# Kernel optimization log

Measured on AMD Instinct MI355X. Metric: run time of the kernel, lower is better.

## Reference

```python
import jax, jax.numpy as jnp
import numpy as np

N = 20000   # nodes
E = 160000  # edges
D = 128     # out_dim == in_dim
H = 8       # heads
DK = D // H # 16


def setup_inputs() -> dict:
    key = jax.random.key(0)
    ks = jax.random.split(key, 16)
    f = lambda i, shape, s=1.0: jax.random.normal(ks[i], shape, dtype=jnp.float32) * s
    z = lambda shape: jnp.zeros(shape, dtype=jnp.float32)
    return {
        "x_txt": f(0, (N, D)), "x_img": f(1, (N, D)), "x_s": f(2, (N, D)),
        "Wk": f(3, (D, D), 0.05), "bk": z((D,)),
        "Wq": f(4, (D, D), 0.05), "bq": z((D,)),
        "Wv": f(5, (D, D), 0.05), "bv": z((D,)),
        "Wa": f(6, (D, D), 0.05), "ba": z((D,)),
        "rel_att": f(7, (H, DK, DK), 0.25),
        "rel_msg": f(8, (H, DK, DK), 0.25),
        "rel_pri": jnp.ones((H,), jnp.float32),
        "wm_txt": f(9, (H, DK, DK), 0.25),
        "wm_img": f(10, (H, DK, DK), 0.25),
        "wm_s": f(11, (H, DK, DK), 0.25),
        "skip": jnp.ones((1,), jnp.float32),
        "src": jax.random.randint(ks[12], (E,), 0, N),
        "dst": jax.random.randint(ks[13], (E,), 0, N),
    }


def reference(x_txt, x_img, x_s, Wk, bk, Wq, bq, Wv, bv, Wa, ba,
              rel_att, rel_msg, rel_pri, wm_txt, wm_img, wm_s, skip, src, dst):
    n_heads, dk = rel_att.shape[0], rel_att.shape[1]
    n_nodes = x_txt.shape[0]
    sqrt_dk = jnp.sqrt(jnp.asarray(dk, jnp.float32))

    def proj(x, W, b):
        return (x @ W + b).reshape(n_nodes, n_heads, dk)

    xs = (x_txt, x_img, x_s)
    k = [proj(x, Wk, bk)[src] for x in xs]  # [E,H,dk] gathered at src
    q = [proj(x, Wq, bq)[dst] for x in xs]  # [E,H,dk] gathered at dst
    v = [proj(x, Wv, bv)[src] for x in xs]

    # cross-modal lambda: per-edge modality alignment softmax (over the 3 modalities)
    wm = (wm_txt, wm_img, wm_s)
    lam_scores = jnp.stack(
        [jnp.einsum('ehd,hdf,ehf->eh', k[m], wm[m], q[m]) for m in range(3)], axis=0)
    lam = jax.nn.softmax(lam_scores, axis=0)  # [3,E,H]

    # edge attention logits (scaled *10 as in reduce_func) and relation-msg values
    att = [jnp.einsum('ehd,hdf,ehf->eh', k[m], rel_att, q[m]) * rel_pri / sqrt_dk * 10.0
           for m in range(3)]
    vmsg = [jnp.einsum('ehd,hdf->ehf', v[m], rel_msg) for m in range(3)]

    align = -(jnp.abs(att[0] - att[1]) + jnp.abs(att[0] - att[2])
              + jnp.abs(att[1] - att[2])) / 3.0

    def seg_softmax(x):  # softmax over edges sharing the same dst node
        m = jax.ops.segment_max(x, dst, num_segments=n_nodes)
        m = jnp.where(jnp.isfinite(m), m, 0.0)
        e = jnp.exp(x - m[dst])
        s = jax.ops.segment_sum(e, dst, num_segments=n_nodes)
        s = jnp.where(s == 0.0, 1.0, s)
        return e / s[dst]

    beta2 = seg_softmax(align)
    sm = [seg_softmax(a) for a in att]
    beta1 = sm[0] * lam[0] + sm[1] * lam[1] + sm[2] * lam[2]
    beta = seg_softmax(beta1 * beta2)  # [E,H]

    alpha = jax.nn.sigmoid(skip)  # [1]
    outs = []
    for m in range(3):
        h = jax.ops.segment_sum(beta[..., None] * vmsg[m], dst,
                                num_segments=n_nodes).reshape(n_nodes, -1)
        outs.append((h @ Wa + ba) * alpha + xs[m] * (1.0 - alpha))
    return tuple(outs)
```

## Files before the change

### kernel.cpp

```cpp
#include <hip/hip_runtime.h>

#define D 128
#define NH 8

typedef __bf16 bf16x8 __attribute__((ext_vector_type(8)));
typedef unsigned short ushortx8 __attribute__((ext_vector_type(8)));
typedef float floatx4 __attribute__((ext_vector_type(4)));

__device__ __forceinline__ float bf2f(unsigned short u) {
  union { unsigned int i; float f; } x; x.i = ((unsigned int)u) << 16; return x.f;
}
__device__ __forceinline__ unsigned short f2bf(float f) {
  union { float f; unsigned int i; } x; x.f = f;
  unsigned int i = x.i;
  return (unsigned short)((i + 0x7FFFu + ((i >> 16) & 1u)) >> 16);
}
__device__ __forceinline__ void acc2(unsigned int ku, unsigned int qu, float& s) {
  union { unsigned int i; float f; } a, b;
  a.i = ku << 16;          b.i = qu << 16;          s += a.f * b.f;
  a.i = ku & 0xffff0000u;  b.i = qu & 0xffff0000u;  s += a.f * b.f;
}

__device__ __forceinline__ void gbar(int* cnt, int nb) {
  __threadfence();
  __syncthreads();
  if (threadIdx.x == 0) {
    __hip_atomic_fetch_add(cnt, 1, __ATOMIC_ACQ_REL, __HIP_MEMORY_SCOPE_AGENT);
    while (__hip_atomic_load(cnt, __ATOMIC_ACQUIRE, __HIP_MEMORY_SCOPE_AGENT) < nb) {}
  }
  __syncthreads();
  __threadfence();
}

__device__ __forceinline__ void fold_item(
    int gid,
    const float* __restrict__ Wk, const float* __restrict__ bk,
    const float* __restrict__ Wq, const float* __restrict__ bq,
    const float* __restrict__ Wv, const float* __restrict__ bv,
    const float* __restrict__ rel_att, const float* __restrict__ rel_msg,
    const float* __restrict__ rel_pri,
    const float* __restrict__ wm0, const float* __restrict__ wm1,
    const float* __restrict__ wm2,
    unsigned short* __restrict__ Wt_all, float* __restrict__ bias_all)
{
  int p = gid >> 14;
  int idx = gid & 16383;
  int c = idx >> 7, k = idx & 127;
  int h = c >> 4, r = c & 15;
  float wsum = 0.f, bsum = 0.f;
  if (p == 0) {
    wsum = Wk[k * 128 + c];
    bsum = bk[c];
  } else if (p <= 4) {
    const float* M = (p == 1) ? rel_att : ((p == 2) ? wm0 : ((p == 3) ? wm1 : wm2));
#pragma unroll
    for (int f = 0; f < 16; f++) {
      float mv = M[h * 256 + r * 16 + f];
      wsum += Wq[k * 128 + h * 16 + f] * mv;
      bsum += bq[h * 16 + f] * mv;
    }
    if (p == 1) { float sc = rel_pri[h] * 2.5f; wsum *= sc; bsum *= sc; }
  } else {
#pragma unroll
    for (int d = 0; d < 16; d++) {
      float mv = rel_msg[h * 256 + d * 16 + r];
      wsum += Wv[k * 128 + h * 16 + d] * mv;
      bsum += bv[h * 16 + d] * mv;
    }
  }
  Wt_all[(size_t)p * 16384 + c * 128 + k] = f2bf(wsum);
  if (k == 0) bias_all[p * 128 + c] = bsum;
}

__device__ __forceinline__ void proj_tile(
    int t, const float* __restrict__ x0, const float* __restrict__ x1,
    const float* __restrict__ x2,
    const unsigned short* __restrict__ Wt_all, const float* __restrict__ bias_all,
    unsigned short* __restrict__ P, int N, unsigned short* Wt, int tid)
{
  int m = t % 3, rt = t / 3;
  const float* X = (m == 0) ? x0 : ((m == 1) ? x1 : x2);
  int wave = tid >> 6, lane = tid & 63;
  int quad = lane >> 4, l16 = lane & 15;
  int row0 = rt * 64 + wave * 16;
  int arow = row0 + l16; if (arow >= N) arow = N - 1;
  const float* ap = X + (size_t)arow * D;
  bf16x8 afr[4];
#pragma unroll
  for (int kk4 = 0; kk4 < 4; kk4++) {
    float4 f0 = *(const float4*)(ap + kk4 * 32 + quad * 8);
    float4 f1 = *(const float4*)(ap + kk4 * 32 + quad * 8 + 4);
    ushortx8 uu;
    uu[0]=f2bf(f0.x); uu[1]=f2bf(f0.y); uu[2]=f2bf(f0.z); uu[3]=f2bf(f0.w);
    uu[4]=f2bf(f1.x); uu[5]=f2bf(f1.y); uu[6]=f2bf(f1.z); uu[7]=f2bf(f1.w);
    afr[kk4] = __builtin_bit_cast(bf16x8, uu);
  }
  for (int pt = 0; pt < 4; pt++) {
    int wp = (pt == 0) ? 0 : ((pt == 1) ? 1 : ((pt == 2) ? (2 + m) : 5));
    const unsigned short* Wsrc = Wt_all + (size_t)wp * 16384;
    const float* B = bias_all + wp * 128;
    floatx4 acc[8];
#pragma unroll
    for (int ct = 0; ct < 8; ct++) acc[ct] = (floatx4)0.f;
    for (int half = 0; half < 2; half++) {
      __syncthreads();
#pragma unroll
      for (int it = 0; it < 4; it++) {
        int idx = it * 256 + tid;
        int c = idx >> 4, kc = (idx & 15) << 3;
        *(uint4*)(&Wt[c * 136 + kc]) =
            *(const uint4*)(&Wsrc[(half * 64 + c) * 128 + kc]);
      }
      __syncthreads();
#pragma unroll
      for (int kk4 = 0; kk4 < 4; kk4++) {
#pragma unroll
        for (int ct2 = 0; ct2 < 4; ct2++) {
          uint4 bu = *(const uint4*)(&Wt[(ct2 * 16 + l16) * 136 + kk4 * 32 + quad * 8]);
          bf16x8 bf = __builtin_bit_cast(bf16x8, bu);
          acc[half * 4 + ct2] =
              __builtin_amdgcn_mfma_f32_16x16x32_bf16(afr[kk4], bf, acc[half * 4 + ct2], 0, 0, 0);
        }
      }
    }
    unsigned short* Pout = P + (size_t)(pt * 3 + m) * N * D;
#pragma unroll
    for (int ct = 0; ct < 8; ct++) {
      int col = ct * 16 + l16;
      float bias = B[col];
#pragma unroll
      for (int i = 0; i < 4; i++) {
        int r = row0 + quad * 4 + i;
        if (r < N) Pout[(size_t)r * D + col] = f2bf(acc[ct][i] + bias);
      }
    }
  }
}

__device__ __forceinline__ void assign_chunk(
    int a, const int* __restrict__ counts, int* __restrict__ row_start,
    int* __restrict__ cursor, int* __restrict__ allocg, int N, int lane)
{
  int n = a * 64 + lane;
  int cnt = (n < N) ? counts[n] : 0;
  int x = cnt;
#pragma unroll
  for (int off = 1; off < 64; off <<= 1) {
    int y = __shfl_up(x, off, 64);
    if (lane >= off) x += y;
  }
  int wtot = __shfl(x, 63, 64);
  int wbase = 0;
  if (lane == 63) wbase = atomicAdd(allocg, wtot);
  wbase = __shfl(wbase, 63, 64);
  if (n < N) { int v = wbase + x - cnt; row_start[n] = v; cursor[n] = v; }
}

__device__ __forceinline__ void edge_vals(
    const unsigned short* __restrict__ P, size_t Nsz, int s, int h,
    const uint4 (&qa)[3][2], const uint4 (&qw)[3][2],
    float (&av)[3], float (&lv)[3])
{
#pragma unroll
  for (int m = 0; m < 3; m++) {
    const unsigned short* kp = P + ((size_t)m * Nsz + s) * 128 + h * 16;
    uint4 k0 = *(const uint4*)kp, k1 = *(const uint4*)(kp + 8);
    const unsigned int* ka = (const unsigned int*)&k0;
    const unsigned int* kb = (const unsigned int*)&k1;
    const unsigned int* a0 = (const unsigned int*)&qa[m][0];
    const unsigned int* a1 = (const unsigned int*)&qa[m][1];
    const unsigned int* w0 = (const unsigned int*)&qw[m][0];
    const unsigned int* w1 = (const unsigned int*)&qw[m][1];
    float da = 0.f, dw = 0.f;
#pragma unroll
    for (int j = 0; j < 4; j++) {
      acc2(ka[j], a0[j], da); acc2(kb[j], a1[j], da);
      acc2(ka[j], w0[j], dw); acc2(kb[j], w1[j], dw);
    }
    av[m] = da;
    lv[m] = dw;
  }
  float mx = fmaxf(lv[0], fmaxf(lv[1], lv[2]));
  float e0 = __expf(lv[0] - mx), e1 = __expf(lv[1] - mx), e2 = __expf(lv[2] - mx);
  float inv = 1.f / (e0 + e1 + e2);
  lv[0] = e0 * inv; lv[1] = e1 * inv; lv[2] = e2 * inv;
}

__device__ __forceinline__ void node_one(
    int n, const unsigned short* __restrict__ P,
    const int* __restrict__ row_start, const int* __restrict__ counts,
    const int* __restrict__ srcs, unsigned short* __restrict__ hagg,
    int N, int lane)
{
  int ro = row_start[n];
  int deg = counts[n];
  float acc00 = 0, acc01 = 0, acc10 = 0, acc11 = 0, acc20 = 0, acc21 = 0;
  if (deg > 0) {
    int h = lane & 7, slot = lane >> 3;
    size_t Nsz = (size_t)N;
    uint4 qa[3][2], qw[3][2];
#pragma unroll
    for (int m = 0; m < 3; m++) {
      const unsigned short* qap = P + ((size_t)(3 + m) * Nsz + n) * 128 + h * 16;
      const unsigned short* qwp = P + ((size_t)(6 + m) * Nsz + n) * 128 + h * 16;
      qa[m][0] = *(const uint4*)qap; qa[m][1] = *(const uint4*)(qap + 8);
      qw[m][0] = *(const uint4*)qwp; qw[m][1] = *(const uint4*)(qwp + 8);
    }
    int nch = (deg + 7) >> 3;
    float cX0[4] = {}, cX1[4] = {}, cX2[4] = {}, cEa[4] = {}, cT[4] = {};
    int cS[4] = {};
    float sA0 = 0, sA1 = 0, sA2 = 0, sAl = 0;
#pragma unroll
    for (int c = 0; c < 4; c++) {
      int idx = c * 8 + slot;
      if (c < nch && idx < deg) {
        int s = srcs[ro + idx]; cS[c] = s;
        float av[3], lv[3];
        edge_vals(P, Nsz, s, h, qa, qw, av, lv);
        float e0 = __expf(av[0]), e1 = __expf(av[1]), e2 = __expf(av[2]);
        float align = -(fabsf(av[0]-av[1]) + fabsf(av[0]-av[2]) + fabsf(av[1]-av[2])) * (1.f/3.f);
        float ea = __expf(align);
        cX0[c] = lv[0] * e0; cX1[c] = lv[1] * e1; cX2[c] = lv[2] * e2; cEa[c] = ea;
        sA0 += e0; sA1 += e1; sA2 += e2; sAl += ea;
      }
    }
    for (int c = 4; c < nch; c++) {
      int idx = c * 8 + slot;
      if (idx < deg) {
        int s = srcs[ro + idx];
        float av[3], lv[3];
        edge_vals(P, Nsz, s, h, qa, qw, av, lv);
        float align = -(fabsf(av[0]-av[1]) + fabsf(av[0]-av[2]) + fabsf(av[1]-av[2])) * (1.f/3.f);
        sA0 += __expf(av[0]); sA1 += __expf(av[1]); sA2 += __expf(av[2]);
        sAl += __expf(align);
      }
    }
#pragma unroll
    for (int off = 8; off < 64; off <<= 1) {
      sA0 += __shfl_xor(sA0, off, 64);
      sA1 += __shfl_xor(sA1, off, 64);
      sA2 += __shfl_xor(sA2, off, 64);
      sAl += __shfl_xor(sAl, off, 64);
    }
    float rA0 = 1.f / fmaxf(sA0, 1e-30f), rA1 = 1.f / fmaxf(sA1, 1e-30f);
    float rA2 = 1.f / fmaxf(sA2, 1e-30f), rAl = 1.f / fmaxf(sAl, 1e-30f);
    float sT = 0;
#pragma unroll
    for (int c = 0; c < 4; c++) {
      int idx = c * 8 + slot;
      if (c < nch && idx < deg) {
        float t = (cX0[c] * rA0 + cX1[c] * rA1 + cX2[c] * rA2) * (cEa[c] * rAl);
        cT[c] = t;
        sT += __expf(t);
      }
    }
    for (int c = 4; c < nch; c++) {
      int idx = c * 8 + slot;
      if (idx < deg) {
        int s = srcs[ro + idx];
        float av[3], lv[3];
        edge_vals(P, Nsz, s, h, qa, qw, av, lv);
        float align = -(fabsf(av[0]-av[1]) + fabsf(av[0]-av[2]) + fabsf(av[1]-av[2])) * (1.f/3.f);
        float t = (lv[0]*__expf(av[0])*rA0 + lv[1]*__expf(av[1])*rA1 + lv[2]*__expf(av[2])*rA2)
                  * (__expf(align) * rAl);
        sT += __expf(t);
      }
    }
#pragma unroll
    for (int off = 8; off < 64; off <<= 1) sT += __shfl_xor(sT, off, 64);
    float rT = 1.f / fmaxf(sT, 1e-30f);
    const unsigned int* Pu = (const unsigned int*)P;
    int hl = lane >> 3;
#pragma unroll
    for (int c = 0; c < 4; c++) {
      if (c < nch) {
        int idx = c * 8 + slot;
        float beta = (idx < deg) ? __expf(cT[c]) * rT : 0.f;
        int sv = cS[c];
        float bj[8]; int sj[8];
#pragma unroll
        for (int jj = 0; jj < 8; jj++) {
          bj[jj] = __shfl(beta, jj * 8 + hl, 64);
          sj[jj] = __shfl(sv, jj * 8, 64);
        }
#pragma unroll
        for (int jj = 0; jj < 8; jj++) {
          size_t base9 = ((size_t)9 * Nsz + sj[jj]) * 64 + lane;
          unsigned int u0 = Pu[base9];
          unsigned int u1 = Pu[base9 + Nsz * 64];
          unsigned int u2 = Pu[base9 + 2 * Nsz * 64];
          float b = bj[jj];
          acc00 += b * bf2f((unsigned short)u0); acc01 += b * bf2f((unsigned short)(u0 >> 16));
          acc10 += b * bf2f((unsigned short)u1); acc11 += b * bf2f((unsigned short)(u1 >> 16));
          acc20 += b * bf2f((unsigned short)u2); acc21 += b * bf2f((unsigned short)(u2 >> 16));
        }
      }
    }
    for (int c = 4; c < nch; c++) {
      int idx = c * 8 + slot;
      float beta = 0.f; int sv = 0;
      if (idx < deg) {
        sv = srcs[ro + idx];
        float av[3], lv[3];
        edge_vals(P, Nsz, sv, h, qa, qw, av, lv);
        float align = -(fabsf(av[0]-av[1]) + fabsf(av[0]-av[2]) + fabsf(av[1]-av[2])) * (1.f/3.f);
        float t = (lv[0]*__expf(av[0])*rA0 + lv[1]*__expf(av[1])*rA1 + lv[2]*__expf(av[2])*rA2)
                  * (__expf(align) * rAl);
        beta = __expf(t) * rT;
      }
      int jmax = min(8, deg - c * 8);
      for (int jj = 0; jj < jmax; jj++) {
        float b = __shfl(beta, jj * 8 + hl, 64);
        int s = __shfl(sv, jj * 8, 64);
        size_t base9 = ((size_t)9 * Nsz + s) * 64 + lane;
        unsigned int u0 = Pu[base9];
        unsigned int u1 = Pu[base9 + Nsz * 64];
        unsigned int u2 = Pu[base9 + 2 * Nsz * 64];
        acc00 += b * bf2f((unsigned short)u0); acc01 += b * bf2f((unsigned short)(u0 >> 16));
        acc10 += b * bf2f((unsigned short)u1); acc11 += b * bf2f((unsigned short)(u1 >> 16));
        acc20 += b * bf2f((unsigned short)u2); acc21 += b * bf2f((unsigned short)(u2 >> 16));
      }
    }
  }
  unsigned int* ho = (unsigned int*)hagg;
  ho[((size_t)0 * N + n) * 64 + lane] = ((unsigned int)f2bf(acc01) << 16) | f2bf(acc00);
  ho[((size_t)1 * N + n) * 64 + lane] = ((unsigned int)f2bf(acc11) << 16) | f2bf(acc10);
  ho[((size_t)2 * N + n) * 64 + lane] = ((unsigned int)f2bf(acc21) << 16) | f2bf(acc20);
}

__device__ __forceinline__ void out_tile_half(
    int t, int half, const unsigned short* __restrict__ Hagg,
    const float* __restrict__ ba,
    const float* __restrict__ x0, const float* __restrict__ x1,
    const float* __restrict__ x2, float alpha,
    float* __restrict__ out, int N, const unsigned short* Wt, int tid)
{
  int m = t % 3, rt = t / 3;
  const float* X = (m == 0) ? x0 : ((m == 1) ? x1 : x2);
  float oma = 1.f - alpha;
  int wave = tid >> 6, lane = tid & 63;
  int quad = lane >> 4, l16 = lane & 15;
  int row0 = rt * 64 + wave * 16;
  int arow = row0 + l16; if (arow >= N) arow = N - 1;
  const unsigned short* hp = Hagg + ((size_t)m * N + arow) * D;
  floatx4 acc[4];
#pragma unroll
  for (int ct = 0; ct < 4; ct++) acc[ct] = (floatx4)0.f;
#pragma unroll
  for (int kk = 0; kk < 128; kk += 32) {
    uint4 au = *(const uint4*)(hp + kk + quad * 8);
    bf16x8 af = __builtin_bit_cast(bf16x8, au);
#pragma unroll
    for (int ct = 0; ct < 4; ct++) {
      uint4 bu = *(const uint4*)(&Wt[(ct * 16 + l16) * 136 + kk + quad * 8]);
      bf16x8 bf = __builtin_bit_cast(bf16x8, bu);
      acc[ct] = __builtin_amdgcn_mfma_f32_16x16x32_bf16(af, bf, acc[ct], 0, 0, 0);
    }
  }
  float* om = out + (size_t)m * N * D;
#pragma unroll
  for (int ct = 0; ct < 4; ct++) {
    int col = half * 64 + ct * 16 + l16;
    float bias = ba[col];
#pragma unroll
    for (int i = 0; i < 4; i++) {
      int r = row0 + quad * 4 + i;
      if (r < N) {
        om[(size_t)r * D + col] =
            (acc[ct][i] + bias) * alpha + X[(size_t)r * D + col] * oma;
      }
    }
  }
}

__global__ __launch_bounds__(256) void k_mega(
    const float* x0, const float* x1, const float* x2,
    const float* Wk, const float* bk, const float* Wq, const float* bq,
    const float* Wv, const float* bv, const float* Wa, const float* ba,
    const float* rel_att, const float* rel_msg, const float* rel_pri,
    const float* wm0, const float* wm1, const float* wm2,
    const float* skip, const int* src, const int* dst,
    float* out, unsigned short* P, unsigned short* Wt_all, float* bias_all,
    int* bar, int* allocg, int* counts, int* cursor, int* row_start,
    int* src_sorted, unsigned short* hagg, int N, int E)
{
  __shared__ __attribute__((aligned(16))) unsigned short Wt[64 * 136];
  int tid = threadIdx.x, bid = blockIdx.x, NB = gridDim.x;
  int gid = bid * 256 + tid, gstride = NB * 256;
  int wave = tid >> 6, lane = tid & 63;

  for (int i = gid; i < N; i += gstride) counts[i] = 0;
  for (int i = gid; i < 6 * 16384; i += gstride)
    fold_item(i, Wk, bk, Wq, bq, Wv, bv, rel_att, rel_msg, rel_pri,
              wm0, wm1, wm2, Wt_all, bias_all);
  gbar(bar + 0 * 16, NB);

  for (int e = gid; e < E; e += gstride) atomicAdd(&counts[dst[e]], 1);
  int ntiles = ((N + 63) / 64) * 3;
  for (int t = bid; t < ntiles; t += NB)
    proj_tile(t, x0, x1, x2, Wt_all, bias_all, P, N, Wt, tid);
  gbar(bar + 1 * 16, NB);

  int nchunks = (N + 63) / 64;
  for (int a = bid * 4 + wave; a < nchunks; a += NB * 4)
    assign_chunk(a, counts, row_start, cursor, allocg, N, lane);
  gbar(bar + 2 * 16, NB);

  for (int e = gid; e < E; e += gstride) {
    int d = dst[e];
    int pos = atomicAdd(&cursor[d], 1);
    src_sorted[pos] = src[e];
  }
  gbar(bar + 3 * 16, NB);

  int ngroups = (N + 3) / 4;
  for (int g = bid; g < ngroups; g += NB) {
    int n = g * 4 + wave;
    if (n < N) node_one(n, P, row_start, counts, src_sorted, hagg, N, lane);
  }
  gbar(bar + 4 * 16, NB);

  float alpha = 1.f / (1.f + __expf(-skip[0]));
  for (int half = 0; half < 2; half++) {
    __syncthreads();
#pragma unroll
    for (int it = 0; it < 8; it++) {
      int idx = it * 256 + tid;
      int k = idx >> 4;
      int c4 = (idx & 15) << 2;
      float4 w = *(const float4*)(&Wa[k * 128 + half * 64 + c4]);
      Wt[(c4 + 0) * 136 + k] = f2bf(w.x);
      Wt[(c4 + 1) * 136 + k] = f2bf(w.y);
      Wt[(c4 + 2) * 136 + k] = f2bf(w.z);
      Wt[(c4 + 3) * 136 + k] = f2bf(w.w);
    }
    __syncthreads();
    for (int t = bid; t < ntiles; t += NB)
      out_tile_half(t, half, hagg, ba, x0, x1, x2, alpha, out, N, Wt, tid);
  }
}

__global__ __launch_bounds__(256) void fb_misc(
    const float* Wk, const float* bk, const float* Wq, const float* bq,
    const float* Wv, const float* bv,
    const float* rel_att, const float* rel_msg, const float* rel_pri,
    const float* wm0, const float* wm1, const float* wm2,
    unsigned short* Wt_all, float* bias_all,
    const int* dst, int* counts, int E)
{
  int b = blockIdx.x;
  if (b < 384) {
    int g = b * 256 + threadIdx.x;
    if (g < 6 * 16384)
      fold_item(g, Wk, bk, Wq, bq, Wv, bv, rel_att, rel_msg, rel_pri,
                wm0, wm1, wm2, Wt_all, bias_all);
  } else {
    int e = (b - 384) * 256 + threadIdx.x;
    if (e < E) atomicAdd(&counts[dst[e]], 1);
  }
}

__global__ __launch_bounds__(256) void fb_projassign(
    const float* x0, const float* x1, const float* x2,
    const unsigned short* Wt_all, const float* bias_all,
    unsigned short* P, const int* counts, int* row_start, int* cursor,
    int* allocg, int N)
{
  __shared__ __attribute__((aligned(16))) unsigned short Wt[64 * 136];
  int ntiles = ((N + 63) / 64) * 3;
  int b = blockIdx.x;
  if (b < ntiles) {
    proj_tile(b, x0, x1, x2, Wt_all, bias_all, P, N, Wt, threadIdx.x);
  } else {
    int a = (b - ntiles) * 4 + (threadIdx.x >> 6);
    if (a < (N + 63) / 64)
      assign_chunk(a, counts, row_start, cursor, allocg, N, threadIdx.x & 63);
  }
}

__global__ void fb_scatter(const int* dst, const int* src, int* cursor,
                           int* src_sorted, int E) {
  int e = blockIdx.x * 256 + threadIdx.x;
  if (e < E) {
    int d = dst[e];
    int pos = atomicAdd(&cursor[d], 1);
    src_sorted[pos] = src[e];
  }
}

__global__ __launch_bounds__(256) void fb_node(
    const unsigned short* P, const int* row_start, const int* counts,
    const int* srcs, unsigned short* hagg, int N)
{
  int n = blockIdx.x * 4 + (threadIdx.x >> 6);
  if (n < N) node_one(n, P, row_start, counts, srcs, hagg, N, threadIdx.x & 63);
}

__global__ __launch_bounds__(256) void fb_out(
    const unsigned short* Hagg, const float* Wa, const float* ba,
    const float* x0, const float* x1, const float* x2, const float* skip,
    float* out, int N)
{
  __shared__ __attribute__((aligned(16))) unsigned short Wt[64 * 136];
  int tid = threadIdx.x;
  float alpha = 1.f / (1.f + __expf(-skip[0]));
  for (int half = 0; half < 2; half++) {
    __syncthreads();
#pragma unroll
    for (int it = 0; it < 8; it++) {
      int idx = it * 256 + tid;
      int k = idx >> 4;
      int c4 = (idx & 15) << 2;
      float4 w = *(const float4*)(&Wa[k * 128 + half * 64 + c4]);
      Wt[(c4 + 0) * 136 + k] = f2bf(w.x);
      Wt[(c4 + 1) * 136 + k] = f2bf(w.y);
      Wt[(c4 + 2) * 136 + k] = f2bf(w.z);
      Wt[(c4 + 3) * 136 + k] = f2bf(w.w);
    }
    __syncthreads();
    out_tile_half(blockIdx.x, half, Hagg, ba, x0, x1, x2, alpha, out, N, Wt, tid);
  }
}

extern "C" void kernel_launch(void* const* d_in, const int* in_sizes, int n_in,
                              void* d_out, int out_size, void* d_ws, size_t ws_size,
                              hipStream_t stream) {
  const float* x0 = (const float*)d_in[0];
  const float* x1 = (const float*)d_in[1];
  const float* x2 = (const float*)d_in[2];
  const float* Wk = (const float*)d_in[3];
  const float* bk = (const float*)d_in[4];
  const float* Wq = (const float*)d_in[5];
  const float* bq = (const float*)d_in[6];
  const float* Wv = (const float*)d_in[7];
  const float* bv = (const float*)d_in[8];
  const float* Wa = (const float*)d_in[9];
  const float* ba = (const float*)d_in[10];
  const float* rel_att = (const float*)d_in[11];
  const float* rel_msg = (const float*)d_in[12];
  const float* rel_pri = (const float*)d_in[13];
  const float* wm0 = (const float*)d_in[14];
  const float* wm1 = (const float*)d_in[15];
  const float* wm2 = (const float*)d_in[16];
  const float* skip = (const float*)d_in[17];
  const int* src = (const int*)d_in[18];
  const int* dstv = (const int*)d_in[19];
  int N = in_sizes[0] / D;
  int E = in_sizes[18];

  char* wsb = (char*)d_ws;
  size_t off = 0;
  auto alloc_b = [&](size_t bytes) { size_t o = off; off += (bytes + 63) & ~(size_t)63; return o; };
  unsigned short* P         = (unsigned short*)(wsb + alloc_b((size_t)12 * N * D * 2));
  unsigned short* Wt_all    = (unsigned short*)(wsb + alloc_b((size_t)6 * 16384 * 2));
  float*          bias_all  = (float*)(wsb + alloc_b((size_t)6 * 128 * 4));
  int*            ctrl      = (int*)(wsb + alloc_b(((size_t)144 + 2 * N) * 4));
  int*            row_start = (int*)(wsb + alloc_b((size_t)(N + 1) * 4));
  int*            src_sorted= (int*)(wsb + alloc_b((size_t)E * 4));
  unsigned short* hagg      = (unsigned short*)(wsb + alloc_b((size_t)3 * N * D * 2));
  int* bar    = ctrl;
  int* allocg = ctrl + 128;
  int* counts = ctrl + 144;
  int* cursor = ctrl + 144 + N;

  hipMemsetAsync(ctrl, 0, ((size_t)144 + N) * sizeof(int), stream);

  int nbPerCu = 0;
  hipError_t oe = hipOccupancyMaxActiveBlocksPerMultiprocessor(&nbPerCu, k_mega, 256, 0);
  if (oe == hipSuccess && nbPerCu >= 1) {
    int grid = nbPerCu * 256;
    if (grid > 2048) grid = 2048;
    k_mega<<<dim3(grid), 256, 0, stream>>>(
        x0, x1, x2, Wk, bk, Wq, bq, Wv, bv, Wa, ba,
        rel_att, rel_msg, rel_pri, wm0, wm1, wm2, skip, src, dstv,
        (float*)d_out, P, Wt_all, bias_all,
        bar, allocg, counts, cursor, row_start, src_sorted, hagg, N, E);
  } else {
    int ntiles = ((N + 63) / 64) * 3;
    int nchunks = (N + 63) / 64;
    fb_misc<<<dim3(384 + (E + 255) / 256), 256, 0, stream>>>(
        Wk, bk, Wq, bq, Wv, bv, rel_att, rel_msg, rel_pri, wm0, wm1, wm2,
        Wt_all, bias_all, dstv, counts, E);
    fb_projassign<<<dim3(ntiles + (nchunks + 3) / 4), 256, 0, stream>>>(
        x0, x1, x2, Wt_all, bias_all, P, counts, row_start, cursor, allocg, N);
    fb_scatter<<<dim3((E + 255) / 256), 256, 0, stream>>>(
        dstv, src, cursor, src_sorted, E);
    fb_node<<<dim3((N + 3) / 4), 256, 0, stream>>>(
        P, row_start, counts, src_sorted, hagg, N);
    fb_out<<<dim3(ntiles), 256, 0, stream>>>(
        hagg, Wa, ba, x0, x1, x2, skip, (float*)d_out, N);
  }
}
```

Before: 251.9 us.

## Use 768-thread blocks with one persistent block per CU in mega kernel

Raises the block size from 256 to 768 threads (12 waves) so each block processes 192-row projection and output tiles and 12 nodes per group. The shared weight tile is then reused by more waves per LDS load. The persistent grid shrinks from up to 2048 blocks to one block per CU, which reduces grid-barrier participants. The cost is fewer resident waves per CU and coarser load balancing across tiles.

```diff
diff --git a/kernel.cpp b/kernel.cpp
--- a/kernel.cpp
+++ b/kernel.cpp
@@ -2,6 +2,10 @@
 
 #define D 128
 #define NH 8
+
+#define NT 768
+#define NW 12
+#define TROWS (NW * 16)
 
 typedef __bf16 bf16x8 __attribute__((ext_vector_type(8)));
 typedef unsigned short ushortx8 __attribute__((ext_vector_type(8)));
@@ -82,7 +86,7 @@
   const float* X = (m == 0) ? x0 : ((m == 1) ? x1 : x2);
   int wave = tid >> 6, lane = tid & 63;
   int quad = lane >> 4, l16 = lane & 15;
-  int row0 = rt * 64 + wave * 16;
+  int row0 = rt * TROWS + wave * 16;
   int arow = row0 + l16; if (arow >= N) arow = N - 1;
   const float* ap = X + (size_t)arow * D;
   bf16x8 afr[4];
@@ -104,9 +108,7 @@
     for (int ct = 0; ct < 8; ct++) acc[ct] = (floatx4)0.f;
     for (int half = 0; half < 2; half++) {
       __syncthreads();
-#pragma unroll
-      for (int it = 0; it < 4; it++) {
-        int idx = it * 256 + tid;
+      for (int idx = tid; idx < 1024; idx += NT) {
         int c = idx >> 4, kc = (idx & 15) << 3;
         *(uint4*)(&Wt[c * 136 + kc]) =
             *(const uint4*)(&Wsrc[(half * 64 + c) * 128 + kc]);
@@ -340,7 +342,7 @@
   float oma = 1.f - alpha;
   int wave = tid >> 6, lane = tid & 63;
   int quad = lane >> 4, l16 = lane & 15;
-  int row0 = rt * 64 + wave * 16;
+  int row0 = rt * TROWS + wave * 16;
   int arow = row0 + l16; if (arow >= N) arow = N - 1;
   const unsigned short* hp = Hagg + ((size_t)m * N + arow) * D;
   floatx4 acc[4];
@@ -373,7 +375,7 @@
   }
 }
 
-__global__ __launch_bounds__(256) void k_mega(
+__global__ __launch_bounds__(NT) void k_mega(
     const float* x0, const float* x1, const float* x2,
     const float* Wk, const float* bk, const float* Wq, const float* bq,
     const float* Wv, const float* bv, const float* Wa, const float* ba,
@@ -386,7 +388,7 @@
 {
   __shared__ __attribute__((aligned(16))) unsigned short Wt[64 * 136];
   int tid = threadIdx.x, bid = blockIdx.x, NB = gridDim.x;
-  int gid = bid * 256 + tid, gstride = NB * 256;
+  int gid = bid * NT + tid, gstride = NB * NT;
   int wave = tid >> 6, lane = tid & 63;
 
   for (int i = gid; i < N; i += gstride) counts[i] = 0;
@@ -396,13 +398,14 @@
   gbar(bar + 0 * 16, NB);
 
   for (int e = gid; e < E; e += gstride) atomicAdd(&counts[dst[e]], 1);
-  int ntiles = ((N + 63) / 64) * 3;
+  int nrt = (N + TROWS - 1) / TROWS;
+  int ntiles = nrt * 3;
   for (int t = bid; t < ntiles; t += NB)
     proj_tile(t, x0, x1, x2, Wt_all, bias_all, P, N, Wt, tid);
   gbar(bar + 1 * 16, NB);
 
   int nchunks = (N + 63) / 64;
-  for (int a = bid * 4 + wave; a < nchunks; a += NB * 4)
+  for (int a = bid * NW + wave; a < nchunks; a += NB * NW)
     assign_chunk(a, counts, row_start, cursor, allocg, N, lane);
   gbar(bar + 2 * 16, NB);
 
@@ -413,9 +416,9 @@
   }
   gbar(bar + 3 * 16, NB);
 
-  int ngroups = (N + 3) / 4;
+  int ngroups = (N + NW - 1) / NW;
   for (int g = bid; g < ngroups; g += NB) {
-    int n = g * 4 + wave;
+    int n = g * NW + wave;
     if (n < N) node_one(n, P, row_start, counts, src_sorted, hagg, N, lane);
   }
   gbar(bar + 4 * 16, NB);
@@ -423,9 +426,7 @@
   float alpha = 1.f / (1.f + __expf(-skip[0]));
   for (int half = 0; half < 2; half++) {
     __syncthreads();
-#pragma unroll
-    for (int it = 0; it < 8; it++) {
-      int idx = it * 256 + tid;
+    for (int idx = tid; idx < 2048; idx += NT) {
       int k = idx >> 4;
       int c4 = (idx & 15) << 2;
       float4 w = *(const float4*)(&Wa[k * 128 + half * 64 + c4]);
@@ -460,19 +461,20 @@
   }
 }
 
-__global__ __launch_bounds__(256) void fb_projassign(
+__global__ __launch_bounds__(NT) void fb_projassign(
     const float* x0, const float* x1, const float* x2,
     const unsigned short* Wt_all, const float* bias_all,
     unsigned short* P, const int* counts, int* row_start, int* cursor,
     int* allocg, int N)
 {
   __shared__ __attribute__((aligned(16))) unsigned short Wt[64 * 136];
-  int ntiles = ((N + 63) / 64) * 3;
+  int nrt = (N + TROWS - 1) / TROWS;
+  int ntiles = nrt * 3;
   int b = blockIdx.x;
   if (b < ntiles) {
     proj_tile(b, x0, x1, x2, Wt_all, bias_all, P, N, Wt, threadIdx.x);
   } else {
-    int a = (b - ntiles) * 4 + (threadIdx.x >> 6);
+    int a = (b - ntiles) * NW + (threadIdx.x >> 6);
     if (a < (N + 63) / 64)
       assign_chunk(a, counts, row_start, cursor, allocg, N, threadIdx.x & 63);
   }
@@ -488,15 +490,15 @@
   }
 }
 
-__global__ __launch_bounds__(256) void fb_node(
+__global__ __launch_bounds__(NT) void fb_node(
     const unsigned short* P, const int* row_start, const int* counts,
     const int* srcs, unsigned short* hagg, int N)
 {
-  int n = blockIdx.x * 4 + (threadIdx.x >> 6);
+  int n = blockIdx.x * NW + (threadIdx.x >> 6);
   if (n < N) node_one(n, P, row_start, counts, srcs, hagg, N, threadIdx.x & 63);
 }
 
-__global__ __launch_bounds__(256) void fb_out(
+__global__ __launch_bounds__(NT) void fb_out(
     const unsigned short* Hagg, const float* Wa, const float* ba,
     const float* x0, const float* x1, const float* x2, const float* skip,
     float* out, int N)
@@ -506,9 +508,7 @@
   float alpha = 1.f / (1.f + __expf(-skip[0]));
   for (int half = 0; half < 2; half++) {
     __syncthreads();
-#pragma unroll
-    for (int it = 0; it < 8; it++) {
-      int idx = it * 256 + tid;
+    for (int idx = tid; idx < 2048; idx += NT) {
       int k = idx >> 4;
       int c4 = (idx & 15) << 2;
       float4 w = *(const float4*)(&Wa[k * 128 + half * 64 + c4]);
@@ -565,29 +565,32 @@
 
   hipMemsetAsync(ctrl, 0, ((size_t)144 + N) * sizeof(int), stream);
 
+  int numCU = 256;
+  hipDeviceGetAttribute(&numCU, hipDeviceAttributeMultiprocessorCount, 0);
+  if (numCU < 1 || numCU > 1024) numCU = 256;
   int nbPerCu = 0;
-  hipError_t oe = hipOccupancyMaxActiveBlocksPerMultiprocessor(&nbPerCu, k_mega, 256, 0);
+  hipError_t oe = hipOccupancyMaxActiveBlocksPerMultiprocessor(&nbPerCu, k_mega, NT, 0);
   if (oe == hipSuccess && nbPerCu >= 1) {
-    int grid = nbPerCu * 256;
-    if (grid > 2048) grid = 2048;
-    k_mega<<<dim3(grid), 256, 0, stream>>>(
+    int grid = numCU;
+    k_mega<<<dim3(grid), NT, 0, stream>>>(
         x0, x1, x2, Wk, bk, Wq, bq, Wv, bv, Wa, ba,
         rel_att, rel_msg, rel_pri, wm0, wm1, wm2, skip, src, dstv,
         (float*)d_out, P, Wt_all, bias_all,
         bar, allocg, counts, cursor, row_start, src_sorted, hagg, N, E);
   } else {
-    int ntiles = ((N + 63) / 64) * 3;
+    int nrt = (N + TROWS - 1) / TROWS;
+    int ntiles = nrt * 3;
     int nchunks = (N + 63) / 64;
     fb_misc<<<dim3(384 + (E + 255) / 256), 256, 0, stream>>>(
         Wk, bk, Wq, bq, Wv, bv, rel_att, rel_msg, rel_pri, wm0, wm1, wm2,
         Wt_all, bias_all, dstv, counts, E);
-    fb_projassign<<<dim3(ntiles + (nchunks + 3) / 4), 256, 0, stream>>>(
+    fb_projassign<<<dim3(ntiles + (nchunks + NW - 1) / NW), NT, 0, stream>>>(
         x0, x1, x2, Wt_all, bias_all, P, counts, row_start, cursor, allocg, N);
     fb_scatter<<<dim3((E + 255) / 256), 256, 0, stream>>>(
         dstv, src, cursor, src_sorted, E);
-    fb_node<<<dim3((N + 3) / 4), 256, 0, stream>>>(
+    fb_node<<<dim3((N + NW - 1) / NW), NT, 0, stream>>>(
         P, row_start, counts, src_sorted, hagg, N);
-    fb_out<<<dim3(ntiles), 256, 0, stream>>>(
+    fb_out<<<dim3(ntiles), NT, 0, stream>>>(
         hagg, Wa, ba, x0, x1, x2, skip, (float*)d_out, N);
   }
 }
```

Result: slower. 331.0 us (+31.4%).
